# Performance work log

Hardware: AMD Instinct MI355X
Metric: run time of the kernel (lower is better)

Reference implementation:

```python
import jax, jax.numpy as jnp
import numpy as np

DIM = 1024
NUM_HEADS = 16
DIM_HEAD = 64
INNER = NUM_HEADS * DIM_HEAD  # 1024
SCALE = DIM_HEAD ** -0.5


def setup_inputs() -> dict:
    key = jax.random.key(0)
    ks = jax.random.split(key, 8)
    B, SQ, SK = 2, 2048, 4096
    x = jax.random.normal(ks[0], (B, SQ, DIM), dtype=jnp.float32)
    context = jax.random.normal(ks[1], (B, SK, DIM), dtype=jnp.float32)
    # LayerNorm params
    ln_gamma = jnp.ones((DIM,), jnp.float32)
    ln_beta = jnp.zeros((DIM,), jnp.float32)
    # Linear weights, stored as [in, out] so y = x @ W (torch Linear weight transposed)
    w_q = jax.random.normal(ks[2], (DIM, INNER), dtype=jnp.float32) / np.sqrt(DIM)
    w_kv = jax.random.normal(ks[3], (DIM, 2 * INNER), dtype=jnp.float32) / np.sqrt(DIM)
    w_out = jax.random.normal(ks[4], (INNER, DIM), dtype=jnp.float32) / np.sqrt(INNER)
    b_out = jnp.zeros((DIM,), jnp.float32)
    # torch init is 0.0 (tanh(0)=0); use a nonzero value so output/grads are nontrivial
    gate = jnp.array([0.5], jnp.float32)
    return {"x": x, "context": context, "ln_gamma": ln_gamma, "ln_beta": ln_beta,
            "w_q": w_q, "w_kv": w_kv, "w_out": w_out, "b_out": b_out, "gate": gate}


def _layernorm(x, gamma, beta, eps=1e-5):
    mu = jnp.mean(x, axis=-1, keepdims=True)
    var = jnp.mean(jnp.square(x - mu), axis=-1, keepdims=True)
    return (x - mu) * jax.lax.rsqrt(var + eps) * gamma + beta


def reference(x, context, ln_gamma, ln_beta, w_q, w_kv, w_out, b_out, gate):
    B, SQ, _ = x.shape
    SK = context.shape[1]
    xn = _layernorm(x, ln_gamma, ln_beta)
    q = (xn @ w_q).reshape(B, SQ, NUM_HEADS, DIM_HEAD)
    kv = context @ w_kv
    k, v = jnp.split(kv, 2, axis=-1)
    k = k.reshape(B, SK, NUM_HEADS, DIM_HEAD)
    v = v.reshape(B, SK, NUM_HEADS, DIM_HEAD)
    # scores: [B, H, SQ, SK]
    scores = jnp.einsum('bqhd,bkhd->bhqk', q * SCALE, k)
    attn = jax.nn.softmax(scores, axis=-1)
    out = jnp.einsum('bhqk,bkhd->bqhd', attn, v).reshape(B, SQ, INNER)
    out = out @ w_out + b_out
    return out * jnp.tanh(gate[0])
```

## Files before the change

### kernel.cpp

```cpp
#include <hip/hip_runtime.h>
#include <hip/hip_bf16.h>
#include <stdint.h>

#define DIMM  1024
#define NHEAD 16
#define DHEAD 64
#define BB    2
#define SQL   2048
#define SKL   4096
#define KVW   2048
#define NT    (SKL / 64)

typedef __attribute__((ext_vector_type(8))) short short8;
typedef __attribute__((ext_vector_type(4))) float f32x4;
typedef __attribute__((ext_vector_type(4))) unsigned short us4;

typedef const __attribute__((address_space(1))) uint32_t gu32_t;
typedef __attribute__((address_space(3))) uint32_t lu32_t;

#define GLDS16(gp, lp) __builtin_amdgcn_global_load_lds((gu32_t*)(gp), (lu32_t*)(lp), 16, 0, 0)

static __device__ __forceinline__ unsigned short f2bf(float f) {
  union { float f; uint32_t u; } v; v.f = f;
  uint32_t r = v.u + 0x7fffu + ((v.u >> 16) & 1u);
  return (unsigned short)(r >> 16);
}

__global__ __launch_bounds__(256) void k_transpose_cast(const float* __restrict__ in,
                                                        unsigned short* __restrict__ out,
                                                        int K, int N) {
  __shared__ float tile[32][33];
  int n0 = blockIdx.x * 32, k0 = blockIdx.y * 32;
  int tx = threadIdx.x, ty = threadIdx.y;
  #pragma unroll
  for (int i = 0; i < 4; i++)
    tile[ty + i * 8][tx] = in[(size_t)(k0 + ty + i * 8) * N + n0 + tx];
  __syncthreads();
  #pragma unroll
  for (int i = 0; i < 4; i++)
    out[(size_t)(n0 + ty + i * 8) * K + k0 + tx] = f2bf(tile[tx][ty + i * 8]);
}

__global__ __launch_bounds__(256) void k_cast(const float* __restrict__ in,
                                              unsigned short* __restrict__ out) {
  size_t i = (size_t)(blockIdx.x * 256 + threadIdx.x) * 4;
  float4 v = *(const float4*)(in + i);
  us4 o;
  o.x = f2bf(v.x); o.y = f2bf(v.y); o.z = f2bf(v.z); o.w = f2bf(v.w);
  *(us4*)(out + i) = o;
}

__global__ __launch_bounds__(256) void k_ln(const float* __restrict__ x,
                                            const float* __restrict__ gamma,
                                            const float* __restrict__ beta,
                                            unsigned short* __restrict__ out) {
  const int row = blockIdx.x, tid = threadIdx.x;
  const float* xr = x + (size_t)row * DIMM;
  float4 v = *(const float4*)(xr + tid * 4);
  float s = v.x + v.y + v.z + v.w;
  float ss = v.x * v.x + v.y * v.y + v.z * v.z + v.w * v.w;
  #pragma unroll
  for (int m = 1; m < 64; m <<= 1) {
    s += __shfl_xor(s, m);
    ss += __shfl_xor(ss, m);
  }
  __shared__ float red[8];
  const int wid = tid >> 6, lane = tid & 63;
  if (lane == 0) { red[wid] = s; red[4 + wid] = ss; }
  __syncthreads();
  s = red[0] + red[1] + red[2] + red[3];
  ss = red[4] + red[5] + red[6] + red[7];
  float mu = s * (1.0f / DIMM);
  float var = ss * (1.0f / DIMM) - mu * mu;
  float rstd = rsqrtf(var + 1e-5f);
  float4 g = *(const float4*)(gamma + tid * 4);
  float4 bt = *(const float4*)(beta + tid * 4);
  us4 o;
  o.x = f2bf((v.x - mu) * rstd * g.x + bt.x);
  o.y = f2bf((v.y - mu) * rstd * g.y + bt.y);
  o.z = f2bf((v.z - mu) * rstd * g.z + bt.z);
  o.w = f2bf((v.w - mu) * rstd * g.w + bt.w);
  *(us4*)(out + (size_t)row * DIMM + tid * 4) = o;
}

template<int MODE>
__global__ __launch_bounds__(256) void k_gemm_bt(const unsigned short* __restrict__ A,
                                                 const unsigned short* __restrict__ BT,
                                                 void* __restrict__ Cv,
                                                 int M, int N, int K,
                                                 const float* __restrict__ bias,
                                                 const float* __restrict__ gate) {
  __shared__ unsigned short lA[2][128 * 32];
  __shared__ unsigned short lB[2][128 * 32];
  const int tid = threadIdx.x;
  const int wid = tid >> 6, lane = tid & 63;
  const int kg = lane >> 4, lr = lane & 15;
  const int wr = wid >> 1, wc = wid & 1;
  const int im = blockIdx.x, in_ = blockIdx.y;
  const int nt = K >> 5;
  const size_t baseA = (size_t)im * 128 * K;
  const size_t baseB = (size_t)in_ * 128 * K;

  f32x4 acc[4][4];
  #pragma unroll
  for (int m = 0; m < 4; m++)
    #pragma unroll
    for (int n = 0; n < 4; n++) {
      f32x4 z = {0.0f, 0.0f, 0.0f, 0.0f};
      acc[m][n] = z;
    }

  auto GSTAGE = [&](int bufi, int t) {
    int k0 = t << 5;
    #pragma unroll
    for (int j = 0; j < 2; j++) {
      int e = wid * 1024 + j * 512 + lane * 8;
      int row = e >> 5;
      int g = (e >> 3) & 3;
      int col = (g ^ ((row >> 1) & 3)) << 3;
      GLDS16(A + baseA + (size_t)row * K + k0 + col, &lA[bufi][e]);
      GLDS16(BT + baseB + (size_t)row * K + k0 + col, &lB[bufi][e]);
    }
  };

  GSTAGE(0, 0);
  __syncthreads();
  int buf = 0;
  for (int t = 0; t < nt; t++) {
    if (t + 1 < nt) GSTAGE(buf ^ 1, t + 1);
    short8 a[4], b[4];
    #pragma unroll
    for (int m = 0; m < 4; m++) {
      int row = wr * 64 + m * 16 + lr;
      a[m] = *(const short8*)&lA[buf][row * 32 + ((kg ^ ((row >> 1) & 3)) << 3)];
    }
    #pragma unroll
    for (int n = 0; n < 4; n++) {
      int row = wc * 64 + n * 16 + lr;
      b[n] = *(const short8*)&lB[buf][row * 32 + ((kg ^ ((row >> 1) & 3)) << 3)];
    }
    #pragma unroll
    for (int m = 0; m < 4; m++)
      #pragma unroll
      for (int n = 0; n < 4; n++)
        acc[m][n] = __builtin_amdgcn_mfma_f32_16x16x32_bf16(a[m], b[n], acc[m][n], 0, 0, 0);
    __syncthreads();
    buf ^= 1;
  }

  const int r0 = im * 128 + wr * 64;
  const int c0 = in_ * 128 + wc * 64;
  if constexpr (MODE == 0) {
    unsigned short* C = (unsigned short*)Cv;
    #pragma unroll
    for (int m = 0; m < 4; m++)
      #pragma unroll
      for (int n = 0; n < 4; n++)
        #pragma unroll
        for (int j = 0; j < 4; j++)
          C[(size_t)(r0 + m * 16 + kg * 4 + j) * N + c0 + n * 16 + lr] = f2bf(acc[m][n][j]);
  } else {
    float* C = (float*)Cv;
    float gl = tanhf(gate[0]);
    #pragma unroll
    for (int m = 0; m < 4; m++)
      #pragma unroll
      for (int n = 0; n < 4; n++)
        #pragma unroll
        for (int j = 0; j < 4; j++) {
          int col = c0 + n * 16 + lr;
          C[(size_t)(r0 + m * 16 + kg * 4 + j) * N + col] = (acc[m][n][j] + bias[col]) * gl;
        }
  }
}

__global__ __launch_bounds__(256, 4) void k_attn(const unsigned short* __restrict__ Q,
                                                 const unsigned short* __restrict__ KV,
                                                 unsigned short* __restrict__ O) {
  __shared__ unsigned short sK[2][64 * 64];
  __shared__ unsigned short sV[2][64 * 64];
  __shared__ unsigned short sP[4][16 * 64];

  const int tid = threadIdx.x;
  const int wid = tid >> 6, lane = tid & 63;
  const int kg = lane >> 4, lr = lane & 15;
  const int qb = blockIdx.x, bh = blockIdx.y;
  const int b = bh >> 4, h = bh & 15;

  const unsigned short* Qp = Q + (size_t)b * SQL * DIMM + h * DHEAD;
  const unsigned short* Kp = KV + (size_t)b * SKL * KVW + h * DHEAD;
  const unsigned short* Vp = Kp + DIMM;

  const int qr0 = qb * 64 + wid * 16;

  const unsigned short* ksrc[2]; int kdst[2];
  #pragma unroll
  for (int j = 0; j < 2; j++) {
    int e = wid * 1024 + j * 512 + lane * 8;
    int row = e >> 6;
    int col = (((e >> 3) & 7) ^ (row & 7)) << 3;
    ksrc[j] = Kp + (size_t)row * KVW + col;
    kdst[j] = e;
  }
  const unsigned short* vsrc[2]; int vdst[2];
  #pragma unroll
  for (int j = 0; j < 2; j++) {
    int g = tid + j * 256;
    int key = (g >> 5) * 4 + ((g & 7) >> 1);
    int d0v = ((g >> 3) & 3) * 16 + (g & 1) * 8;
    vsrc[j] = Vp + (size_t)key * KVW + d0v;
    vdst[j] = g * 8;
  }

  auto STAGE = [&](int bufi, int kt) {
    size_t off = (size_t)kt * 64 * KVW;
    #pragma unroll
    for (int j = 0; j < 2; j++) GLDS16(ksrc[j] + off, &sK[bufi][kdst[j]]);
    #pragma unroll
    for (int j = 0; j < 2; j++) GLDS16(vsrc[j] + off, &sV[bufi][vdst[j]]);
  };

  short8 qa[2];
  #pragma unroll
  for (int ks = 0; ks < 2; ks++) {
    short8 v = *(const short8*)(Qp + (size_t)(qr0 + lr) * DIMM + ks * 32 + kg * 8);
    #pragma unroll
    for (int j = 0; j < 8; j++) {
      union { float f; uint32_t u; } c;
      c.u = ((uint32_t)(unsigned short)v[j]) << 16;
      v[j] = (short)f2bf(c.f * 0.1803368801111f);
    }
    qa[ks] = v;
  }

  f32x4 oacc[4];
  #pragma unroll
  for (int n = 0; n < 4; n++) {
    f32x4 z = {0.0f, 0.0f, 0.0f, 0.0f};
    oacc[n] = z;
  }
  float rs = 0.0f;

  const uint32_t sVb0 = (uint32_t)(size_t)(lu32_t*)&sV[0][0] + (uint32_t)(kg * 1024 + lr * 8);
  unsigned char* const sPw = (unsigned char*)&sP[wid][0];
  const uint32_t swz = (uint32_t)((lr & 7) << 4);

  STAGE(0, 0);
  __syncthreads();

  int buf = 0;
  for (int kt = 0; kt < NT; kt++) {
    if (kt + 1 < NT) STAGE(buf ^ 1, kt + 1);

    short8 kb[4][2];
    #pragma unroll
    for (int n = 0; n < 4; n++)
      #pragma unroll
      for (int ks = 0; ks < 2; ks++) {
        int row = n * 16 + lr;
        kb[n][ks] = *(const short8*)&sK[buf][row * 64 + (((ks * 4 + kg) ^ (row & 7)) << 3)];
      }
    f32x4 sc[4];
    #pragma unroll
    for (int n = 0; n < 4; n++) {
      f32x4 z = {0.0f, 0.0f, 0.0f, 0.0f};
      sc[n] = z;
    }
    #pragma unroll
    for (int n = 0; n < 4; n++)
      #pragma unroll
      for (int ks = 0; ks < 2; ks++)
        sc[n] = __builtin_amdgcn_mfma_f32_16x16x32_bf16(kb[n][ks], qa[ks], sc[n], 0, 0, 0);

    #pragma unroll
    for (int n = 0; n < 4; n++) {
      float p0 = __builtin_amdgcn_exp2f(sc[n][0]);
      float p1 = __builtin_amdgcn_exp2f(sc[n][1]);
      float p2 = __builtin_amdgcn_exp2f(sc[n][2]);
      float p3 = __builtin_amdgcn_exp2f(sc[n][3]);
      rs += (p0 + p1) + (p2 + p3);
      uint32_t lo, hi;
      asm("v_cvt_pk_bf16_f32 %0, %1, %2" : "=v"(lo) : "v"(p0), "v"(p1));
      asm("v_cvt_pk_bf16_f32 %0, %1, %2" : "=v"(hi) : "v"(p2), "v"(p3));
      uint2 w2; w2.x = lo; w2.y = hi;
      *(uint2*)(sPw + (((uint32_t)(lr * 128 + n * 32 + kg * 8)) ^ swz)) = w2;
    }

    asm volatile("" ::: "memory");

    short8 pa[2];
    #pragma unroll
    for (int ks2 = 0; ks2 < 2; ks2++)
      pa[ks2] = *(const short8*)(sPw + (((uint32_t)(lr * 128 + ks2 * 64 + kg * 16)) ^ swz));

    union { uint4 u; short8 s; } vbu[4][2];
    {
      uint32_t tb = sVb0 + (uint32_t)(buf * 8192);
      #pragma unroll
      for (int n = 0; n < 4; n++)
        #pragma unroll
        for (int ks2 = 0; ks2 < 2; ks2++) {
          uint2 t0, t1;
          uint32_t a0 = tb + (uint32_t)(ks2 * 4096 + n * 128);
          asm volatile("ds_read_b64_tr_b16 %0, %1" : "=v"(t0) : "v"(a0));
          asm volatile("ds_read_b64_tr_b16 %0, %1" : "=v"(t1) : "v"(a0 + 512u));
          vbu[n][ks2].u.x = t0.x; vbu[n][ks2].u.y = t0.y;
          vbu[n][ks2].u.z = t1.x; vbu[n][ks2].u.w = t1.y;
        }
    }
    asm volatile("s_waitcnt lgkmcnt(0)" ::: "memory");
    __builtin_amdgcn_sched_barrier(0);

    #pragma unroll
    for (int n = 0; n < 4; n++)
      #pragma unroll
      for (int ks2 = 0; ks2 < 2; ks2++)
        oacc[n] = __builtin_amdgcn_mfma_f32_16x16x32_bf16(pa[ks2], vbu[n][ks2].s, oacc[n], 0, 0, 0);

    __syncthreads();
    buf ^= 1;
  }

  float t = rs;
  t += __shfl_xor(t, 16);
  t += __shfl_xor(t, 32);
  float inv = 1.0f / t;
  float rq[4];
  #pragma unroll
  for (int j = 0; j < 4; j++)
    rq[j] = __shfl(inv, kg * 4 + j);

  unsigned short* Op = O + (size_t)b * SQL * DIMM + h * DHEAD;
  #pragma unroll
  for (int n = 0; n < 4; n++)
    #pragma unroll
    for (int j = 0; j < 4; j++)
      Op[(size_t)(qr0 + kg * 4 + j) * DIMM + n * 16 + lr] = f2bf(oacc[n][j] * rq[j]);
}

extern "C" void kernel_launch(void* const* d_in, const int* in_sizes, int n_in,
                              void* d_out, int out_size, void* d_ws, size_t ws_size,
                              hipStream_t stream) {
  (void)in_sizes; (void)n_in; (void)out_size; (void)ws_size;
  const float* x     = (const float*)d_in[0];
  const float* ctx   = (const float*)d_in[1];
  const float* gamma = (const float*)d_in[2];
  const float* beta  = (const float*)d_in[3];
  const float* w_q   = (const float*)d_in[4];
  const float* w_kv  = (const float*)d_in[5];
  const float* w_out = (const float*)d_in[6];
  const float* b_out = (const float*)d_in[7];
  const float* gate  = (const float*)d_in[8];
  float* out = (float*)d_out;
  char* ws = (char*)d_ws;

  unsigned short* XN   = (unsigned short*)(ws);
  unsigned short* QB   = (unsigned short*)(ws + (8ull  << 20));
  unsigned short* CTXB = (unsigned short*)(ws + (16ull << 20));
  unsigned short* KVB  = (unsigned short*)(ws + (32ull << 20));
  unsigned short* OB   = (unsigned short*)(ws + (64ull << 20));
  unsigned short* WQT  = (unsigned short*)(ws + (72ull << 20));
  unsigned short* WKVT = (unsigned short*)(ws + (74ull << 20));
  unsigned short* WOT  = (unsigned short*)(ws + (78ull << 20));

  k_transpose_cast<<<dim3(32, 32), dim3(32, 8), 0, stream>>>(w_q, WQT, 1024, 1024);
  k_transpose_cast<<<dim3(64, 32), dim3(32, 8), 0, stream>>>(w_kv, WKVT, 1024, 2048);
  k_transpose_cast<<<dim3(32, 32), dim3(32, 8), 0, stream>>>(w_out, WOT, 1024, 1024);
  k_cast<<<dim3(8192), dim3(256), 0, stream>>>(ctx, CTXB);
  k_ln<<<dim3(4096), dim3(256), 0, stream>>>(x, gamma, beta, XN);
  k_gemm_bt<0><<<dim3(32, 8), dim3(256), 0, stream>>>(XN, WQT, QB, 4096, 1024, 1024, nullptr, nullptr);
  k_gemm_bt<0><<<dim3(64, 16), dim3(256), 0, stream>>>(CTXB, WKVT, KVB, 8192, 2048, 1024, nullptr, nullptr);
  k_attn<<<dim3(32, 32), dim3(256), 0, stream>>>(QB, KVB, OB);
  k_gemm_bt<1><<<dim3(32, 8), dim3(256), 0, stream>>>(OB, WOT, out, 4096, 1024, 1024, b_out, gate);
}
```

Baseline: 235.8 us.

## Switch attention to 32x32x16 MFMA with register-resident P via permlane swaps

Rewrites the attention kernel so each wave handles 32 query rows using 32x32x16 bf16 MFMA instead of 16x16x32. The softmax probabilities are repacked in registers with v_permlane32_swap instead of a round trip through shared memory, and the sP buffer is removed. Blocks shrink to two waves (128 threads), each doing more staging loads. This cuts LDS traffic and raises MFMA work per K/V tile load, at the cost of higher register pressure and fewer waves per block to hide latency.

```diff
diff --git a/kernel.cpp b/kernel.cpp
--- a/kernel.cpp
+++ b/kernel.cpp
@@ -13,6 +13,7 @@
 
 typedef __attribute__((ext_vector_type(8))) short short8;
 typedef __attribute__((ext_vector_type(4))) float f32x4;
+typedef __attribute__((ext_vector_type(16))) float f32x16;
 typedef __attribute__((ext_vector_type(4))) unsigned short us4;
 
 typedef const __attribute__((address_space(1))) uint32_t gu32_t;
@@ -174,16 +175,15 @@
   }
 }
 
-__global__ __launch_bounds__(256, 4) void k_attn(const unsigned short* __restrict__ Q,
-                                                 const unsigned short* __restrict__ KV,
-                                                 unsigned short* __restrict__ O) {
+__global__ __launch_bounds__(128) void k_attn(const unsigned short* __restrict__ Q,
+                                              const unsigned short* __restrict__ KV,
+                                              unsigned short* __restrict__ O) {
   __shared__ unsigned short sK[2][64 * 64];
   __shared__ unsigned short sV[2][64 * 64];
-  __shared__ unsigned short sP[4][16 * 64];
 
   const int tid = threadIdx.x;
   const int wid = tid >> 6, lane = tid & 63;
-  const int kg = lane >> 4, lr = lane & 15;
+  const int l31 = lane & 31, hi = lane >> 5;
   const int qb = blockIdx.x, bh = blockIdx.y;
   const int b = bh >> 4, h = bh & 15;
 
@@ -191,22 +191,19 @@
   const unsigned short* Kp = KV + (size_t)b * SKL * KVW + h * DHEAD;
   const unsigned short* Vp = Kp + DIMM;
 
-  const int qr0 = qb * 64 + wid * 16;
-
-  const unsigned short* ksrc[2]; int kdst[2];
-  #pragma unroll
-  for (int j = 0; j < 2; j++) {
-    int e = wid * 1024 + j * 512 + lane * 8;
+  const int qr0 = qb * 64 + wid * 32;
+
+  const unsigned short* ksrc[4]; int kdst[4];
+  const unsigned short* vsrc[4]; int vdst[4];
+  #pragma unroll
+  for (int j = 0; j < 4; j++) {
+    int e = (tid + j * 128) * 8;
     int row = e >> 6;
     int col = (((e >> 3) & 7) ^ (row & 7)) << 3;
     ksrc[j] = Kp + (size_t)row * KVW + col;
     kdst[j] = e;
-  }
-  const unsigned short* vsrc[2]; int vdst[2];
-  #pragma unroll
-  for (int j = 0; j < 2; j++) {
-    int g = tid + j * 256;
-    int key = (g >> 5) * 4 + ((g & 7) >> 1);
+    int g = tid + j * 128;
+    int key = (g >> 5) * 4 + ((g >> 1) & 3);
     int d0v = ((g >> 3) & 3) * 16 + (g & 1) * 8;
     vsrc[j] = Vp + (size_t)key * KVW + d0v;
     vdst[j] = g * 8;
@@ -215,35 +212,33 @@
   auto STAGE = [&](int bufi, int kt) {
     size_t off = (size_t)kt * 64 * KVW;
     #pragma unroll
-    for (int j = 0; j < 2; j++) GLDS16(ksrc[j] + off, &sK[bufi][kdst[j]]);
-    #pragma unroll
-    for (int j = 0; j < 2; j++) GLDS16(vsrc[j] + off, &sV[bufi][vdst[j]]);
+    for (int j = 0; j < 4; j++) GLDS16(ksrc[j] + off, &sK[bufi][kdst[j]]);
+    #pragma unroll
+    for (int j = 0; j < 4; j++) GLDS16(vsrc[j] + off, &sV[bufi][vdst[j]]);
   };
 
-  short8 qa[2];
-  #pragma unroll
-  for (int ks = 0; ks < 2; ks++) {
-    short8 v = *(const short8*)(Qp + (size_t)(qr0 + lr) * DIMM + ks * 32 + kg * 8);
+  short8 qa[4];
+  #pragma unroll
+  for (int t = 0; t < 4; t++) {
+    short8 v = *(const short8*)(Qp + (size_t)(qr0 + l31) * DIMM + t * 16 + hi * 8);
     #pragma unroll
     for (int j = 0; j < 8; j++) {
       union { float f; uint32_t u; } c;
       c.u = ((uint32_t)(unsigned short)v[j]) << 16;
       v[j] = (short)f2bf(c.f * 0.1803368801111f);
     }
-    qa[ks] = v;
-  }
-
-  f32x4 oacc[4];
-  #pragma unroll
-  for (int n = 0; n < 4; n++) {
-    f32x4 z = {0.0f, 0.0f, 0.0f, 0.0f};
-    oacc[n] = z;
-  }
+    qa[t] = v;
+  }
+
+  f32x16 oacc[2];
+  #pragma unroll
+  for (int d2 = 0; d2 < 2; d2++)
+    #pragma unroll
+    for (int r = 0; r < 16; r++) oacc[d2][r] = 0.0f;
   float rs = 0.0f;
 
-  const uint32_t sVb0 = (uint32_t)(size_t)(lu32_t*)&sV[0][0] + (uint32_t)(kg * 1024 + lr * 8);
-  unsigned char* const sPw = (unsigned char*)&sP[wid][0];
-  const uint32_t swz = (uint32_t)((lr & 7) << 4);
+  const uint32_t sVb0 = (uint32_t)(size_t)(lu32_t*)&sV[0][0] +
+                        (uint32_t)(hi * 1024 + ((lane >> 4) & 1) * 128 + (lane & 15) * 8);
 
   STAGE(0, 0);
   __syncthreads();
@@ -252,90 +247,92 @@
   for (int kt = 0; kt < NT; kt++) {
     if (kt + 1 < NT) STAGE(buf ^ 1, kt + 1);
 
-    short8 kb[4][2];
-    #pragma unroll
-    for (int n = 0; n < 4; n++)
-      #pragma unroll
-      for (int ks = 0; ks < 2; ks++) {
-        int row = n * 16 + lr;
-        kb[n][ks] = *(const short8*)&sK[buf][row * 64 + (((ks * 4 + kg) ^ (row & 7)) << 3)];
+    short8 kbf[2][4];
+    #pragma unroll
+    for (int kb2 = 0; kb2 < 2; kb2++)
+      #pragma unroll
+      for (int t = 0; t < 4; t++) {
+        int row = kb2 * 32 + l31;
+        int gl = t * 2 + hi;
+        kbf[kb2][t] = *(const short8*)&sK[buf][row * 64 + ((gl ^ (row & 7)) << 3)];
       }
-    f32x4 sc[4];
-    #pragma unroll
-    for (int n = 0; n < 4; n++) {
-      f32x4 z = {0.0f, 0.0f, 0.0f, 0.0f};
-      sc[n] = z;
-    }
-    #pragma unroll
-    for (int n = 0; n < 4; n++)
-      #pragma unroll
-      for (int ks = 0; ks < 2; ks++)
-        sc[n] = __builtin_amdgcn_mfma_f32_16x16x32_bf16(kb[n][ks], qa[ks], sc[n], 0, 0, 0);
-
-    #pragma unroll
-    for (int n = 0; n < 4; n++) {
-      float p0 = __builtin_amdgcn_exp2f(sc[n][0]);
-      float p1 = __builtin_amdgcn_exp2f(sc[n][1]);
-      float p2 = __builtin_amdgcn_exp2f(sc[n][2]);
-      float p3 = __builtin_amdgcn_exp2f(sc[n][3]);
-      rs += (p0 + p1) + (p2 + p3);
-      uint32_t lo, hi;
-      asm("v_cvt_pk_bf16_f32 %0, %1, %2" : "=v"(lo) : "v"(p0), "v"(p1));
-      asm("v_cvt_pk_bf16_f32 %0, %1, %2" : "=v"(hi) : "v"(p2), "v"(p3));
-      uint2 w2; w2.x = lo; w2.y = hi;
-      *(uint2*)(sPw + (((uint32_t)(lr * 128 + n * 32 + kg * 8)) ^ swz)) = w2;
-    }
-
-    asm volatile("" ::: "memory");
-
-    short8 pa[2];
-    #pragma unroll
-    for (int ks2 = 0; ks2 < 2; ks2++)
-      pa[ks2] = *(const short8*)(sPw + (((uint32_t)(lr * 128 + ks2 * 64 + kg * 16)) ^ swz));
-
-    union { uint4 u; short8 s; } vbu[4][2];
+
+    union u4s8 { uint32_t u[4]; short8 s; };
+    u4s8 paf[4];
+    #pragma unroll
+    for (int kb2 = 0; kb2 < 2; kb2++) {
+      f32x16 sc;
+      #pragma unroll
+      for (int r = 0; r < 16; r++) sc[r] = 0.0f;
+      #pragma unroll
+      for (int t = 0; t < 4; t++)
+        sc = __builtin_amdgcn_mfma_f32_32x32x16_bf16(kbf[kb2][t], qa[t], sc, 0, 0, 0);
+
+      float p[16];
+      #pragma unroll
+      for (int r = 0; r < 16; r++) {
+        p[r] = __builtin_amdgcn_exp2f(sc[r]);
+        rs += p[r];
+      }
+      uint32_t w[8];
+      #pragma unroll
+      for (int i = 0; i < 8; i++)
+        asm("v_cvt_pk_bf16_f32 %0, %1, %2" : "=v"(w[i]) : "v"(p[2 * i]), "v"(p[2 * i + 1]));
+      asm("v_permlane32_swap_b32 %0, %1" : "+v"(w[0]), "+v"(w[2]));
+      asm("v_permlane32_swap_b32 %0, %1" : "+v"(w[1]), "+v"(w[3]));
+      asm("v_permlane32_swap_b32 %0, %1" : "+v"(w[4]), "+v"(w[6]));
+      asm("v_permlane32_swap_b32 %0, %1" : "+v"(w[5]), "+v"(w[7]));
+      paf[kb2 * 2].u[0] = w[0]; paf[kb2 * 2].u[1] = w[1];
+      paf[kb2 * 2].u[2] = w[2]; paf[kb2 * 2].u[3] = w[3];
+      paf[kb2 * 2 + 1].u[0] = w[4]; paf[kb2 * 2 + 1].u[1] = w[5];
+      paf[kb2 * 2 + 1].u[2] = w[6]; paf[kb2 * 2 + 1].u[3] = w[7];
+    }
+
+    u4s8 vb[2][4];
     {
       uint32_t tb = sVb0 + (uint32_t)(buf * 8192);
       #pragma unroll
-      for (int n = 0; n < 4; n++)
+      for (int d2 = 0; d2 < 2; d2++)
         #pragma unroll
-        for (int ks2 = 0; ks2 < 2; ks2++) {
+        for (int ks = 0; ks < 4; ks++) {
           uint2 t0, t1;
-          uint32_t a0 = tb + (uint32_t)(ks2 * 4096 + n * 128);
+          uint32_t a0 = tb + (uint32_t)(d2 * 256 + ks * 2048);
           asm volatile("ds_read_b64_tr_b16 %0, %1" : "=v"(t0) : "v"(a0));
           asm volatile("ds_read_b64_tr_b16 %0, %1" : "=v"(t1) : "v"(a0 + 512u));
-          vbu[n][ks2].u.x = t0.x; vbu[n][ks2].u.y = t0.y;
-          vbu[n][ks2].u.z = t1.x; vbu[n][ks2].u.w = t1.y;
+          vb[d2][ks].u[0] = t0.x; vb[d2][ks].u[1] = t0.y;
+          vb[d2][ks].u[2] = t1.x; vb[d2][ks].u[3] = t1.y;
         }
     }
     asm volatile("s_waitcnt lgkmcnt(0)" ::: "memory");
     __builtin_amdgcn_sched_barrier(0);
 
     #pragma unroll
-    for (int n = 0; n < 4; n++)
-      #pragma unroll
-      for (int ks2 = 0; ks2 < 2; ks2++)
-        oacc[n] = __builtin_amdgcn_mfma_f32_16x16x32_bf16(pa[ks2], vbu[n][ks2].s, oacc[n], 0, 0, 0);
+    for (int d2 = 0; d2 < 2; d2++)
+      #pragma unroll
+      for (int ks = 0; ks < 4; ks++)
+        oacc[d2] = __builtin_amdgcn_mfma_f32_32x32x16_bf16(paf[ks].s, vb[d2][ks].s, oacc[d2], 0, 0, 0);
 
     __syncthreads();
     buf ^= 1;
   }
 
-  float t = rs;
-  t += __shfl_xor(t, 16);
-  t += __shfl_xor(t, 32);
+  float t = rs + __shfl_xor(rs, 32);
   float inv = 1.0f / t;
-  float rq[4];
-  #pragma unroll
-  for (int j = 0; j < 4; j++)
-    rq[j] = __shfl(inv, kg * 4 + j);
+  float rq[16];
+  #pragma unroll
+  for (int r = 0; r < 16; r++) {
+    int rho = (r & 3) + 8 * (r >> 2) + 4 * hi;
+    rq[r] = __shfl(inv, rho);
+  }
 
   unsigned short* Op = O + (size_t)b * SQL * DIMM + h * DHEAD;
   #pragma unroll
-  for (int n = 0; n < 4; n++)
-    #pragma unroll
-    for (int j = 0; j < 4; j++)
-      Op[(size_t)(qr0 + kg * 4 + j) * DIMM + n * 16 + lr] = f2bf(oacc[n][j] * rq[j]);
+  for (int d2 = 0; d2 < 2; d2++)
+    #pragma unroll
+    for (int r = 0; r < 16; r++) {
+      int rho = (r & 3) + 8 * (r >> 2) + 4 * hi;
+      Op[(size_t)(qr0 + rho) * DIMM + d2 * 32 + l31] = f2bf(oacc[d2][r] * rq[r]);
+    }
 }
 
 extern "C" void kernel_launch(void* const* d_in, const int* in_sizes, int n_in,
@@ -370,6 +367,6 @@
   k_ln<<<dim3(4096), dim3(256), 0, stream>>>(x, gamma, beta, XN);
   k_gemm_bt<0><<<dim3(32, 8), dim3(256), 0, stream>>>(XN, WQT, QB, 4096, 1024, 1024, nullptr, nullptr);
   k_gemm_bt<0><<<dim3(64, 16), dim3(256), 0, stream>>>(CTXB, WKVT, KVB, 8192, 2048, 1024, nullptr, nullptr);
-  k_attn<<<dim3(32, 32), dim3(256), 0, stream>>>(QB, KVB, OB);
+  k_attn<<<dim3(32, 32), dim3(128), 0, stream>>>(QB, KVB, OB);
   k_gemm_bt<1><<<dim3(32, 8), dim3(256), 0, stream>>>(OB, WOT, out, 4096, 1024, 1024, b_out, gate);
 }
```

Result: slower. 257.3 us (+9.1%).
